# Performance work log

Measured on AMD Instinct MI355X. Metric: run time of the kernel, lower is better.

## Reference

```python
import jax, jax.numpy as jnp
import numpy as np


def conv(x, w, b=None, pad=1):
    y = jax.lax.conv_general_dilated(x, w, (1, 1), [(pad, pad), (pad, pad)],
                                     dimension_numbers=('NCHW', 'OIHW', 'NCHW'))
    if b is not None:
        y = y + b[None, :, None, None]
    return y


def grid_sample(img, gx, gy):
    # bilinear, zeros padding, align_corners=False (torch F.grid_sample default)
    B, C, H, W = img.shape
    ix = ((gx + 1.0) * W - 1.0) * 0.5
    iy = ((gy + 1.0) * H - 1.0) * 0.5
    x0 = jnp.floor(ix)
    y0 = jnp.floor(iy)

    def gather(xi, yi):
        valid = (xi >= 0) & (xi <= W - 1) & (yi >= 0) & (yi <= H - 1)
        xc = jnp.clip(xi, 0, W - 1).astype(jnp.int32)
        yc = jnp.clip(yi, 0, H - 1).astype(jnp.int32)
        b = jnp.arange(B)[:, None, None]
        return img[b, :, yc, xc] * valid[..., None].astype(img.dtype)  # (B,H,W,C)

    wx1 = ix - x0
    wy1 = iy - y0
    wx0 = 1.0 - wx1
    wy0 = 1.0 - wy1
    out = (gather(x0, y0) * (wx0 * wy0)[..., None]
           + gather(x0 + 1, y0) * (wx1 * wy0)[..., None]
           + gather(x0, y0 + 1) * (wx0 * wy1)[..., None]
           + gather(x0 + 1, y0 + 1) * (wx1 * wy1)[..., None])
    return out.transpose(0, 3, 1, 2)  # (B,C,H,W)


def setup_inputs() -> dict:
    key = jax.random.key(0)
    ks = jax.random.split(key, 32)
    B, H, W, hd = 4, 512, 512, 16
    f = lambda k, shp: jax.random.normal(k, shp, dtype=jnp.float32) * 0.05
    z = lambda n: jnp.zeros((n,), dtype=jnp.float32)
    d = {
        'net': f(ks[0], (B, hd, H, W)),
        'inp': f(ks[1], (B, hd, H, W)),
        'corr': f(ks[2], (B, 3, H, W)),
        'noise': f(ks[3], (B, 3, H, W)),
        # BasicMotionEncoder (channels=3, hidden=32, output_dim=64)
        'wc1': f(ks[4], (32, 3, 3, 3)), 'bc1': z(32),
        'wc2': f(ks[5], (32, 32, 3, 3)), 'bc2': z(32),
        'wf1': f(ks[6], (32, 3, 3, 3)), 'bf1': z(32),
        'wf2': f(ks[7], (32, 32, 3, 3)), 'bf2': z(32),
        'we': f(ks[8], (61, 64, 3, 3)), 'be': z(61),
        # SepConvGRU (hidden_size=16, L=4)
        'loc1_w': f(ks[9], (16, 96, 5, 5)), 'loc1_b': z(16),
        'loc2_w': f(ks[10], (8, 16, 5, 5)), 'loc2_b': z(8),
        'wz': f(ks[11], (16, 144, 3, 3)), 'bz': z(16),
        'wr': f(ks[12], (16, 144, 3, 3)), 'br': z(16),
        'wq': f(ks[13], (16, 96, 3, 3)), 'bq': z(16),
        # CBAM (reduction 16 -> mid=1; bias-free, standard impl)
        'ca_w1': f(ks[14], (1, 16, 1, 1)),
        'ca_w2': f(ks[15], (16, 1, 1, 1)),
        'sa_w': f(ks[16], (1, 2, 7, 7)),
        # FlowHead (input 16, hidden 64, out 3)
        'fh1_w': f(ks[17], (64, 16, 3, 3)), 'fh1_b': z(64),
        'fh2_w': f(ks[18], (3, 64, 3, 3)), 'fh2_b': z(3),
    }
    return d


def reference(net, inp, corr, noise, wc1, bc1, wc2, bc2, wf1, bf1, wf2, bf2, we, be,
              loc1_w, loc1_b, loc2_w, loc2_b, wz, bz, wr, br, wq, bq,
              ca_w1, ca_w2, sa_w, fh1_w, fh1_b, fh2_w, fh2_b):
    # --- BasicMotionEncoder ---
    cor = jax.nn.relu(conv(corr, wc1, bc1, 1))
    cor = jax.nn.relu(conv(cor, wc2, bc2, 1))
    flo = jax.nn.relu(conv(noise, wf1, bf1, 1))
    flo = jax.nn.relu(conv(flo, wf2, bf2, 1))
    mo = jax.nn.relu(conv(jnp.concatenate([cor, flo], 1), we, be, 1))
    motion = jnp.concatenate([mo, noise], 1)  # (B,64,H,W)
    x = jnp.concatenate([inp, motion], 1)     # (B,hd+64,H,W)
    h = net
    B, C, H, W = h.shape
    # --- SepConvGRU ---
    t = jax.nn.leaky_relu(conv(jnp.concatenate([x, h], 1), loc1_w, loc1_b, 2), 0.2)
    flows = conv(t, loc2_w, loc2_b, 2)        # (B,2L,H,W)
    L = flows.shape[1] // 2
    flows = flows.reshape(B, L, 2, H, W)
    xx = jnp.arange(W, dtype=h.dtype)[None, None, :]  # (1,1,W)
    yy = jnp.arange(H, dtype=h.dtype)[None, :, None]  # (1,H,1)

    def warp_one(flow):  # flow: (B,2,H,W); warp h by -flow
        vgx = xx - flow[:, 0]
        vgy = yy - flow[:, 1]
        gx = 2.0 * vgx / max(W - 1, 1) - 1.0
        gy = 2.0 * vgy / max(H - 1, 1) - 1.0
        return grid_sample(h, gx, gy)

    wrapped = jax.vmap(warp_one, in_axes=1, out_axes=1)(flows)  # (B,L,C,H,W)
    wrapped = wrapped.reshape(B, L * C, H, W)
    hx = jnp.concatenate([wrapped, x], 1)     # (B,9*hd,H,W)
    zg = jax.nn.sigmoid(conv(hx, wz, bz, 1))
    rg = jax.nn.sigmoid(conv(hx, wr, br, 1))
    q = jnp.tanh(conv(jnp.concatenate([rg * h, x], 1), wq, bq, 1))
    h = (1.0 - zg) * h + zg * q
    # --- CBAM ---
    avg = h.mean((2, 3), keepdims=True)
    mx = h.max((2, 3), keepdims=True)
    mlp = lambda v: conv(jax.nn.relu(conv(v, ca_w1, None, 0)), ca_w2, None, 0)
    h = h * jax.nn.sigmoid(mlp(avg) + mlp(mx))
    sa = jnp.concatenate([h.mean(1, keepdims=True), h.max(1, keepdims=True)], 1)
    h = h * jax.nn.sigmoid(conv(sa, sa_w, None, 3))
    # --- FlowHead ---
    delta_flow = conv(jax.nn.relu(conv(h, fh1_w, fh1_b, 1)), fh2_w, fh2_b, 1)
    return h, delta_flow
```

## Files before the change

### kernel.cpp

```cpp
#include <hip/hip_runtime.h>
#include <hip/hip_bf16.h>
#include <math.h>

using bf16 = __hip_bfloat16;
typedef __attribute__((ext_vector_type(8))) short short8;
typedef __attribute__((ext_vector_type(4))) float f32x4;

__device__ __forceinline__ float b2f(bf16 v){ return __bfloat162float(v); }
__device__ __forceinline__ bf16 f2b(float v){ return __float2bfloat16(v); }
__device__ __forceinline__ float bs2f(short s){
  union{unsigned u; float f;} x; x.u = ((unsigned)(unsigned short)s)<<16; return x.f;
}

template<int A> __device__ __forceinline__ float act_fn(float v){
  if constexpr (A==1) return fmaxf(v, 0.f);
  else if constexpr (A==2) return v > 0.f ? v : 0.2f*v;
  else if constexpr (A==3) return 1.f/(1.f+expf(-v));
  else if constexpr (A==4) return tanhf(v);
  else return v;
}

struct Srcs9 { const bf16* p[9]; int code[9]; };
struct WMap  { int base[9]; int lo[9]; int hi[9]; };

template<int KK, int ACT, int NT>
__global__ __launch_bounds__(256) void conv_mfma(
    Srcs9 S, int Gin, const bf16* __restrict__ flows,
    const bf16* __restrict__ Bw, const float* __restrict__ bias,
    bf16* __restrict__ outS, size_t slabS, float* __restrict__ outF, int Cout,
    int H, int W)
{
  constexpr int TS=16, HALO=TS+KK-1, PAD=KK/2, NPAIR=(KK*KK+1)/2, HH=HALO*HALO;
  constexpr int NMT = (NT==1)?4:((NT==2)?8:16);
  __shared__ __align__(16) bf16 As[2][HH*24];
  const int tid=threadIdx.x, lane=tid&63, wv=tid>>6;
  const int ln=lane&15, gq=lane>>4;
  const int tilesx=W/TS;
  const int tx0=(blockIdx.x%tilesx)*TS, ty0=(blockIdx.x/tilesx)*TS;
  const int b=blockIdx.z; const int HW=H*W;
  int ntile, mt0;
  if constexpr (NT==1){ ntile=0;    mt0=wv*4; }
  else if constexpr (NT==2){ ntile=wv&1; mt0=(wv>>1)*8; }
  else { ntile=wv; mt0=0; }

  f32x4 acc[NMT];
  #pragma unroll
  for (int t=0;t<NMT;++t) acc[t]=(f32x4){0.f,0.f,0.f,0.f};

  const short8 Z8 = {0,0,0,0,0,0,0,0};
  const int px0=tid, px1=tid+256;
  const int hy0=px0/HALO, hx0=px0-hy0*HALO;
  const int hy1=px1/HALO, hx1=px1-hy1*HALO;
  const bool act1 = (px1<HH);
  const int gy0=ty0+hy0-PAD, gx0=tx0+hx0-PAD;
  const int gy1=ty0+hy1-PAD, gx1=tx0+hx1-PAD;
  const bool in0 = (gy0>=0&&gy0<H&&gx0>=0&&gx0<W);
  const bool in1 = act1 && (gy1>=0&&gy1<H&&gx1>=0&&gx1<W);

  auto gather = [&](int g, bool inb, int gy, int gx, short8& A0, short8& A1){
    const int code = S.code[g];
    const bf16* sp = S.p[g];
    if (code == 0) {
      if (inb) {
        const bf16* qp = sp + ((size_t)b*HW + (size_t)gy*W + gx)*16;
        A0 = *(const short8*)qp; A1 = *(const short8*)(qp+8);
      } else { A0 = Z8; A1 = Z8; }
    } else {
      if (inb) {
        const int l = code-1;
        const size_t p = (size_t)b*HW + (size_t)gy*W + gx;
        const unsigned fp_ = *(const unsigned*)(flows + p*16 + 2*l);
        const float fx = bs2f((short)(fp_&0xffff)), fy = bs2f((short)(fp_>>16));
        const float vgx = (float)gx - fx, vgy = (float)gy - fy;
        const float gxn = 2.f*vgx/(float)(W-1) - 1.f;
        const float gyn = 2.f*vgy/(float)(H-1) - 1.f;
        const float ix = ((gxn+1.f)*(float)W - 1.f)*0.5f;
        const float iy = ((gyn+1.f)*(float)H - 1.f)*0.5f;
        const float x0f = floorf(ix), y0f = floorf(iy);
        const float wx1 = ix-x0f, wy1 = iy-y0f, wx0 = 1.f-wx1, wy0 = 1.f-wy1;
        const int x0=(int)x0f, y0=(int)y0f, x1=x0+1, y1=y0+1;
        const bool vx0=(x0>=0)&(x0<W), vx1=(x1>=0)&(x1<W);
        const bool vy0=(y0>=0)&(y0<H), vy1=(y1>=0)&(y1<H);
        const int xc0=min(max(x0,0),W-1), xc1=min(max(x1,0),W-1);
        const int yc0=min(max(y0,0),H-1), yc1=min(max(y1,0),H-1);
        const float w00=wx0*wy0*((vx0&&vy0)?1.f:0.f);
        const float w10=wx1*wy0*((vx1&&vy0)?1.f:0.f);
        const float w01=wx0*wy1*((vx0&&vy1)?1.f:0.f);
        const float w11=wx1*wy1*((vx1&&vy1)?1.f:0.f);
        const bf16* nb = sp + (size_t)b*HW*16;
        const bf16* p00 = nb + ((size_t)yc0*W+xc0)*16;
        const bf16* p10 = nb + ((size_t)yc0*W+xc1)*16;
        const bf16* p01 = nb + ((size_t)yc1*W+xc0)*16;
        const bf16* p11 = nb + ((size_t)yc1*W+xc1)*16;
        const short8 a00=*(const short8*)p00, b00=*(const short8*)(p00+8);
        const short8 a10=*(const short8*)p10, b10=*(const short8*)(p10+8);
        const short8 a01=*(const short8*)p01, b01=*(const short8*)(p01+8);
        const short8 a11=*(const short8*)p11, b11=*(const short8*)(p11+8);
        __align__(16) bf16 tmp[16];
        #pragma unroll
        for (int c=0;c<8;++c){
          tmp[c]   = f2b(w00*bs2f(a00[c]) + w10*bs2f(a10[c]) + w01*bs2f(a01[c]) + w11*bs2f(a11[c]));
          tmp[8+c] = f2b(w00*bs2f(b00[c]) + w10*bs2f(b10[c]) + w01*bs2f(b01[c]) + w11*bs2f(b11[c]));
        }
        A0 = *(const short8*)tmp; A1 = *(const short8*)(tmp+8);
      } else { A0 = Z8; A1 = Z8; }
    }
  };

  auto mfma_g = [&](int g, const bf16* buf){
    #pragma unroll
    for (int p=0;p<NPAIR;++p){
      const short8 bfrag = *(const short8*)(Bw + ((((size_t)g*NPAIR+p)*NT + ntile)*64 + lane)*8);
      int off = 2*p + (gq>>1);
      if (off >= KK*KK) off = 0;
      const int dy = off/KK, dx = off - (off/KK)*KK;
      const int ce = (ln+dx)*24 + ((gq&1)*8);
      #pragma unroll
      for (int t=0;t<NMT;++t){
        const short8 af = *(const short8*)(buf + (size_t)(mt0+t+dy)*HALO*24 + ce);
        acc[t] = __builtin_amdgcn_mfma_f32_16x16x32_bf16(af, bfrag, acc[t], 0, 0, 0);
      }
    }
  };

  for (int g=0; g<Gin; ++g) {
    short8 a0, a1, c0v, c1v;
    gather(g, in0, gy0, gx0, a0, a1);
    if (act1) gather(g, in1, gy1, gx1, c0v, c1v);
    if (g > 0) mfma_g(g-1, As[(g-1)&1]);
    bf16* buf = As[g&1];
    *(short8*)(buf + (size_t)px0*24)     = a0;
    *(short8*)(buf + (size_t)px0*24 + 8) = a1;
    if (act1){
      *(short8*)(buf + (size_t)px1*24)     = c0v;
      *(short8*)(buf + (size_t)px1*24 + 8) = c1v;
    }
    __syncthreads();
  }
  mfma_g(Gin-1, As[(Gin-1)&1]);

  const int co = ntile*16 + ln;
  const float bv = bias[co];
  if (outS) {
    #pragma unroll
    for (int t=0;t<NMT;++t){
      const int y = ty0 + mt0 + t;
      bf16* op = outS + (size_t)ntile*slabS + ((size_t)b*HW + (size_t)y*W + tx0 + gq*4)*16 + ln;
      #pragma unroll
      for (int r=0;r<4;++r) op[(size_t)r*16] = f2b(act_fn<ACT>(acc[t][r] + bv));
    }
  } else {
    if (co < Cout) {
      #pragma unroll
      for (int t=0;t<NMT;++t){
        const int y = ty0 + mt0 + t;
        float4 f;
        f.x = act_fn<ACT>(acc[t][0]+bv); f.y = act_fn<ACT>(acc[t][1]+bv);
        f.z = act_fn<ACT>(acc[t][2]+bv); f.w = act_fn<ACT>(acc[t][3]+bv);
        *(float4*)(outF + ((size_t)b*Cout + co)*HW + (size_t)y*W + tx0 + gq*4) = f;
      }
    }
  }
}

__global__ void prep_w(const float* __restrict__ W1, const float* __restrict__ W2, int coSplit,
                       const float* __restrict__ b1, const float* __restrict__ b2,
                       WMap M, int NPAIR, int NTp, int Cout, int CinO, int T,
                       bf16* __restrict__ Bw, float* __restrict__ bOut, int total)
{
  const int i = blockIdx.x*256 + threadIdx.x;
  if (i < total) {
    const int j=i&7, l=(i>>3)&63, ln2=l&15, gq2=l>>4;
    int r=i>>9; const int nt=r%NTp; r/=NTp; const int p=r%NPAIR; const int g=r/NPAIR;
    const int k=gq2*8+j, off=2*p+(k>>4), ci=k&15, co=nt*16+ln2;
    float w=0.f;
    if (off<T && co<Cout && ci>=M.lo[g] && ci<M.hi[g]) {
      const int cin = M.base[g]+ci;
      if (!W2 || co<coSplit) w = W1[((size_t)co*CinO+cin)*T+off];
      else                   w = W2[((size_t)(co-coSplit)*CinO+cin)*T+off];
    }
    Bw[i] = f2b(w);
  }
  if (i < 64) {
    float bv=0.f;
    if (i<Cout) bv = (!b2 || i<coSplit) ? (b1? b1[i]:0.f) : b2[i-coSplit];
    bOut[i]=bv;
  }
}

__global__ void pack16(const float* __restrict__ src, bf16* __restrict__ dst, int HW){
  const int px = blockIdx.x*256+threadIdx.x; const int b=blockIdx.y;
  if (px>=HW) return;
  __align__(16) bf16 t[16];
  #pragma unroll
  for (int c=0;c<16;++c) t[c]=f2b(src[((size_t)b*16+c)*HW+px]);
  bf16* d = dst + ((size_t)b*HW+px)*16;
  *(short8*)d = *(const short8*)t; *(short8*)(d+8) = *(const short8*)(t+8);
}

__global__ void pack_cn(const float* __restrict__ corr, const float* __restrict__ noise,
                        bf16* __restrict__ dst, int HW){
  const int px = blockIdx.x*256+threadIdx.x; const int b=blockIdx.y;
  if (px>=HW) return;
  __align__(16) bf16 t[16];
  #pragma unroll
  for (int c=0;c<16;++c) t[c]=f2b(0.f);
  #pragma unroll
  for (int c=0;c<3;++c){
    t[c]   = f2b(corr [((size_t)b*3+c)*HW+px]);
    t[3+c] = f2b(noise[((size_t)b*3+c)*HW+px]);
  }
  bf16* d = dst + ((size_t)b*HW+px)*16;
  *(short8*)d = *(const short8*)t; *(short8*)(d+8) = *(const short8*)(t+8);
}

__global__ void noise_tail(const float* __restrict__ noise, bf16* __restrict__ mslab3, int HW){
  const int px = blockIdx.x*256+threadIdx.x; const int b=blockIdx.y;
  if (px>=HW) return;
  bf16* d = mslab3 + ((size_t)b*HW+px)*16;
  #pragma unroll
  for (int c=0;c<3;++c) d[13+c] = f2b(noise[((size_t)b*3+c)*HW+px]);
}

__global__ void rh_k(const bf16* __restrict__ rg, const bf16* __restrict__ netT,
                     bf16* __restrict__ rh, int HW){
  const int px = blockIdx.x*256+threadIdx.x; const int b=blockIdx.y;
  if (px>=HW) return;
  const size_t base = ((size_t)b*HW+px)*16;
  const short8 r0=*(const short8*)(rg+base),  r1=*(const short8*)(rg+base+8);
  const short8 n0=*(const short8*)(netT+base), n1=*(const short8*)(netT+base+8);
  __align__(16) bf16 t[16];
  #pragma unroll
  for (int c=0;c<8;++c){
    t[c]   = f2b(bs2f(r0[c])*bs2f(n0[c]));
    t[8+c] = f2b(bs2f(r1[c])*bs2f(n1[c]));
  }
  *(short8*)(rh+base) = *(const short8*)t; *(short8*)(rh+base+8) = *(const short8*)(t+8);
}

__global__ void h1_k(const bf16* __restrict__ zg, const bf16* __restrict__ q,
                     const float* __restrict__ net, bf16* __restrict__ hT, int HW){
  const int px = blockIdx.x*256+threadIdx.x; const int b=blockIdx.y;
  if (px>=HW) return;
  const size_t base = ((size_t)b*HW+px)*16;
  const short8 z0=*(const short8*)(zg+base), z1=*(const short8*)(zg+base+8);
  const short8 q0=*(const short8*)(q+base),  q1=*(const short8*)(q+base+8);
  __align__(16) bf16 t[16];
  #pragma unroll
  for (int c=0;c<8;++c){
    const float za=bs2f(z0[c]), zb=bs2f(z1[c]);
    const float na=net[((size_t)b*16+c)*HW+px], nb2=net[((size_t)b*16+8+c)*HW+px];
    t[c]   = f2b((1.f-za)*na + za*bs2f(q0[c]));
    t[8+c] = f2b((1.f-zb)*nb2 + zb*bs2f(q1[c]));
  }
  *(short8*)(hT+base) = *(const short8*)t; *(short8*)(hT+base+8) = *(const short8*)(t+8);
}

__global__ __launch_bounds__(256) void castats_p1(const bf16* __restrict__ hT,
                                                  float* __restrict__ part, int HW){
  const int blk=blockIdx.x, b=blockIdx.y;
  const int per = HW>>5;
  const bf16* base = hT + ((size_t)b*HW + (size_t)blk*per)*16;
  float s[16], m[16];
  #pragma unroll
  for (int c=0;c<16;++c){ s[c]=0.f; m[c]=-3.4e38f; }
  for (int i=threadIdx.x;i<per;i+=256){
    const short8 a=*(const short8*)(base+(size_t)i*16);
    const short8 bb=*(const short8*)(base+(size_t)i*16+8);
    #pragma unroll
    for (int c=0;c<8;++c){
      const float v=bs2f(a[c]);  s[c]+=v;   m[c]=fmaxf(m[c],v);
      const float w=bs2f(bb[c]); s[8+c]+=w; m[8+c]=fmaxf(m[8+c],w);
    }
  }
  #pragma unroll
  for (int o=32;o>=1;o>>=1){
    #pragma unroll
    for (int c=0;c<16;++c){ s[c]+=__shfl_down(s[c],o); m[c]=fmaxf(m[c],__shfl_down(m[c],o)); }
  }
  __shared__ float ls[4][16], lm[4][16];
  const int w4=threadIdx.x>>6;
  if ((threadIdx.x&63)==0){
    #pragma unroll
    for (int c=0;c<16;++c){ ls[w4][c]=s[c]; lm[w4][c]=m[c]; }
  }
  __syncthreads();
  if (threadIdx.x<16){
    const int c=threadIdx.x;
    part[((size_t)(b*32+blk))*32 + c]      = ls[0][c]+ls[1][c]+ls[2][c]+ls[3][c];
    part[((size_t)(b*32+blk))*32 + 16 + c] = fmaxf(fmaxf(lm[0][c],lm[1][c]),fmaxf(lm[2][c],lm[3][c]));
  }
}

__global__ void castats_p2(const float* __restrict__ part, float* __restrict__ stats, int HW){
  const int t = threadIdx.x; if (t>=64) return;
  const int b=t>>4, c=t&15;
  float s=0.f, m=-3.4e38f;
  for (int k=0;k<32;++k){
    s += part[((size_t)(b*32+k))*32 + c];
    m  = fmaxf(m, part[((size_t)(b*32+k))*32 + 16 + c]);
  }
  stats[t*2]=s/(float)HW; stats[t*2+1]=m;
}

__global__ void cascale_k(const float* __restrict__ stats, const float* __restrict__ w1,
                          const float* __restrict__ w2, float* __restrict__ scale){
  const int t = threadIdx.x; if (t>=64) return;
  const int c = t & 15;
  float pa = w1[c]*stats[t*2], pm = w1[c]*stats[t*2+1];
  #pragma unroll
  for (int o=8;o>=1;o>>=1){ pa += __shfl_xor(pa,o,16); pm += __shfl_xor(pm,o,16); }
  const float y = w2[c]*fmaxf(pa,0.f) + w2[c]*fmaxf(pm,0.f);
  scale[t] = 1.f/(1.f+expf(-y));
}

__global__ void sastats_k(const bf16* __restrict__ hT, const float* __restrict__ scale,
                          bf16* __restrict__ sa2, int HW){
  const int px = blockIdx.x*256+threadIdx.x; const int b=blockIdx.y;
  if (px>=HW) return;
  const size_t base = ((size_t)b*HW+px)*16;
  const short8 a=*(const short8*)(hT+base), c8=*(const short8*)(hT+base+8);
  float s=0.f, m=-3.4e38f;
  #pragma unroll
  for (int c=0;c<8;++c){
    const float v=bs2f(a[c])*scale[b*16+c];    s+=v; m=fmaxf(m,v);
    const float w=bs2f(c8[c])*scale[b*16+8+c]; s+=w; m=fmaxf(m,w);
  }
  sa2[((size_t)b*2+0)*HW+px] = f2b(s*(1.f/16.f));
  sa2[((size_t)b*2+1)*HW+px] = f2b(m);
}

__global__ __launch_bounds__(256) void saconv_k(const bf16* __restrict__ sa2,
    const float* __restrict__ w, bf16* __restrict__ samap, int H, int W){
  __shared__ float wl[98];
  if (threadIdx.x < 98) wl[threadIdx.x] = w[threadIdx.x];
  __syncthreads();
  const int i = blockIdx.x*256 + threadIdx.x; const int b = blockIdx.y;
  const int HW = H*W;
  if (i >= HW) return;
  const int y = i / W, x = i - (i/W)*W;
  float s = 0.f;
  #pragma unroll
  for (int ch=0; ch<2; ++ch){
    const size_t base = ((size_t)b*2+ch)*HW;
    for (int ky=0;ky<7;++ky){
      const int yy=y+ky-3; if (yy<0||yy>=H) continue;
      for (int kx=0;kx<7;++kx){
        const int xx=x+kx-3; if (xx<0||xx>=W) continue;
        s += b2f(sa2[base+(size_t)yy*W+xx]) * wl[ch*49+ky*7+kx];
      }
    }
  }
  samap[(size_t)b*HW+i] = f2b(1.f/(1.f+expf(-s)));
}

__global__ void hfinal_k(bf16* __restrict__ hT, const float* __restrict__ scale,
                         const bf16* __restrict__ samap, float* __restrict__ outh, int HW){
  const int px = blockIdx.x*256+threadIdx.x; const int b=blockIdx.y;
  if (px>=HW) return;
  const float sa = b2f(samap[(size_t)b*HW+px]);
  const size_t base = ((size_t)b*HW+px)*16;
  const short8 a=*(const short8*)(hT+base), c8=*(const short8*)(hT+base+8);
  __align__(16) bf16 t[16];
  #pragma unroll
  for (int c=0;c<8;++c){
    const float v=bs2f(a[c])*scale[b*16+c]*sa;
    const float w=bs2f(c8[c])*scale[b*16+8+c]*sa;
    t[c]=f2b(v); t[8+c]=f2b(w);
    outh[((size_t)b*16+c)*HW+px]=v; outh[((size_t)b*16+8+c)*HW+px]=w;
  }
  *(short8*)(hT+base)=*(const short8*)t; *(short8*)(hT+base+8)=*(const short8*)(t+8);
}

extern "C" void kernel_launch(void* const* d_in, const int* in_sizes, int n_in,
                              void* d_out, int out_size, void* d_ws, size_t ws_size,
                              hipStream_t stream)
{
  const float* net   = (const float*)d_in[0];
  const float* inp   = (const float*)d_in[1];
  const float* corr  = (const float*)d_in[2];
  const float* noise = (const float*)d_in[3];
  const float* wc1 = (const float*)d_in[4];  const float* bc1 = (const float*)d_in[5];
  const float* wc2 = (const float*)d_in[6];  const float* bc2 = (const float*)d_in[7];
  const float* wf1 = (const float*)d_in[8];  const float* bf1 = (const float*)d_in[9];
  const float* wf2 = (const float*)d_in[10]; const float* bf2 = (const float*)d_in[11];
  const float* we  = (const float*)d_in[12]; const float* be  = (const float*)d_in[13];
  const float* loc1_w = (const float*)d_in[14]; const float* loc1_b = (const float*)d_in[15];
  const float* loc2_w = (const float*)d_in[16]; const float* loc2_b = (const float*)d_in[17];
  const float* wz = (const float*)d_in[18]; const float* bz = (const float*)d_in[19];
  const float* wr = (const float*)d_in[20]; const float* br = (const float*)d_in[21];
  const float* wq = (const float*)d_in[22]; const float* bq = (const float*)d_in[23];
  const float* ca_w1 = (const float*)d_in[24]; const float* ca_w2 = (const float*)d_in[25];
  const float* sa_w  = (const float*)d_in[26];
  const float* fh1_w = (const float*)d_in[27]; const float* fh1_b = (const float*)d_in[28];
  const float* fh2_w = (const float*)d_in[29]; const float* fh2_b = (const float*)d_in[30];

  const int B = 4, H = 512, W = 512, HW = H*W;
  const size_t U  = 32ull<<20;
  const size_t SS = (size_t)B*HW*16;
  char* ws = (char*)d_ws;

  bf16* cor1   = (bf16*)(ws + 0*U);
  bf16* flo1   = (bf16*)(ws + 2*U);
  bf16* flo2   = (bf16*)(ws + 4*U);
  bf16* cnoise = (bf16*)(ws + 6*U);
  bf16* motion = (bf16*)(ws + 0*U);
  bf16* inpT   = (bf16*)(ws + 4*U);
  bf16* tbuf   = (bf16*)(ws + 5*U);
  bf16* netT   = (bf16*)(ws + 6*U);
  bf16* flows  = (bf16*)(ws + 7*U);
  bf16* rh     = (bf16*)(ws + 5*U);
  bf16* qb     = (bf16*)(ws + 6*U);
  bf16* hT     = (bf16*)(ws + 5*U);
  bf16* fh1o   = (bf16*)(ws + 0*U);
  float* part    = (float*)(ws + 4*U);
  float* stats   = (float*)(ws + 4*U + (64<<10));
  float* scale   = (float*)(ws + 4*U + (128<<10));
  bf16*  sa2     = (bf16*)(ws + 4*U + (1<<20));
  bf16*  samap   = (bf16*)(ws + 4*U + (6<<20));
  bf16*  Bw_fh2  = (bf16*)(ws + 4*U + (16<<20));
  float* bias_fh2= (float*)(ws + 4*U + (17<<20));

  float* out_h  = (float*)d_out;
  float* out_df = out_h + (size_t)B*16*HW;
  bf16*  cor2   = (bf16*)d_out;
  bf16*  zgrg   = (bf16*)d_out;
  bf16*  BwAll  = (bf16*)out_df;
  float* biasAll= (float*)(BwAll + 190464);

  const size_t oCor1=0, oCor2=5120, oFlo1=15360, oFlo2=20480, oMo=30720,
               oLoc1=71680, oLoc2=111616, oZgrg=118272, oQ=164352, oFh1=179712;

  const dim3 pgrid((HW+255)/256, B);
  const dim3 cgrid((W/16)*(H/16), 1, B);

  auto WM = [](int b0,int b1,int b2,int b3,int b4,int b5,int b6,int b7,int b8,
               int lo0,int hi0)->WMap{
    WMap m{};
    const int bs[9]={b0,b1,b2,b3,b4,b5,b6,b7,b8};
    for (int g=0; g<9; ++g){ m.base[g]=bs[g]; m.lo[g]=0; m.hi[g]=16; }
    m.lo[0]=lo0; m.hi[0]=hi0;
    return m;
  };

  #define PREP(W1,W2,SPL,B1,B2,MAP,NP,NTP,CO,CIN,T,BWOFF,BIDX) \
    { const int tot = 0; (void)tot; \
      const int total = ((BWOFF##_G)*(NP)*(NTP))*512; \
      prep_w<<<(total+255)/256,256,0,stream>>>(W1,W2,SPL,B1,B2,MAP,NP,NTP,CO,CIN,T, \
        BwAll+BWOFF, biasAll+BIDX*64, total); }

  { const int G=1, NP=5, NTP=2, total=G*NP*NTP*512;
    prep_w<<<(total+255)/256,256,0,stream>>>(wc1,nullptr,0,bc1,nullptr,
      WM(0,0,0,0,0,0,0,0,0, 0,3), NP,NTP,32,3,9, BwAll+oCor1, biasAll+0*64, total); }
  { const int G=2, NP=5, NTP=2, total=G*NP*NTP*512;
    prep_w<<<(total+255)/256,256,0,stream>>>(wc2,nullptr,0,bc2,nullptr,
      WM(0,16,0,0,0,0,0,0,0, 0,16), NP,NTP,32,32,9, BwAll+oCor2, biasAll+1*64, total); }
  { const int G=1, NP=5, NTP=2, total=G*NP*NTP*512;
    prep_w<<<(total+255)/256,256,0,stream>>>(wf1,nullptr,0,bf1,nullptr,
      WM(-3,0,0,0,0,0,0,0,0, 3,6), NP,NTP,32,3,9, BwAll+oFlo1, biasAll+2*64, total); }
  { const int G=2, NP=5, NTP=2, total=G*NP*NTP*512;
    prep_w<<<(total+255)/256,256,0,stream>>>(wf2,nullptr,0,bf2,nullptr,
      WM(0,16,0,0,0,0,0,0,0, 0,16), NP,NTP,32,32,9, BwAll+oFlo2, biasAll+3*64, total); }
  { const int G=4, NP=5, NTP=4, total=G*NP*NTP*512;
    prep_w<<<(total+255)/256,256,0,stream>>>(we,nullptr,0,be,nullptr,
      WM(0,16,32,48,0,0,0,0,0, 0,16), NP,NTP,61,64,9, BwAll+oMo, biasAll+4*64, total); }
  { const int G=6, NP=13, NTP=1, total=G*NP*NTP*512;
    prep_w<<<(total+255)/256,256,0,stream>>>(loc1_w,nullptr,0,loc1_b,nullptr,
      WM(0,16,32,48,64,80,0,0,0, 0,16), NP,NTP,16,96,25, BwAll+oLoc1, biasAll+5*64, total); }
  { const int G=1, NP=13, NTP=1, total=G*NP*NTP*512;
    prep_w<<<(total+255)/256,256,0,stream>>>(loc2_w,nullptr,0,loc2_b,nullptr,
      WM(0,0,0,0,0,0,0,0,0, 0,16), NP,NTP,8,16,25, BwAll+oLoc2, biasAll+6*64, total); }
  { const int G=9, NP=5, NTP=2, total=G*NP*NTP*512;
    prep_w<<<(total+255)/256,256,0,stream>>>(wz,wr,16,bz,br,
      WM(0,16,32,48,64,80,96,112,128, 0,16), NP,NTP,32,144,9, BwAll+oZgrg, biasAll+7*64, total); }
  { const int G=6, NP=5, NTP=1, total=G*NP*NTP*512;
    prep_w<<<(total+255)/256,256,0,stream>>>(wq,nullptr,0,bq,nullptr,
      WM(0,16,32,48,64,80,0,0,0, 0,16), NP,NTP,16,96,9, BwAll+oQ, biasAll+8*64, total); }
  { const int G=1, NP=5, NTP=4, total=G*NP*NTP*512;
    prep_w<<<(total+255)/256,256,0,stream>>>(fh1_w,nullptr,0,fh1_b,nullptr,
      WM(0,0,0,0,0,0,0,0,0, 0,16), NP,NTP,64,16,9, BwAll+oFh1, biasAll+9*64, total); }

  pack_cn<<<pgrid,256,0,stream>>>(corr, noise, cnoise, HW);
  { Srcs9 S{}; S.p[0]=cnoise; S.code[0]=0;
    conv_mfma<3,1,2><<<cgrid,256,0,stream>>>(S,1,nullptr,BwAll+oCor1,biasAll+0*64,cor1,SS,nullptr,32,H,W); }
  { Srcs9 S{}; S.p[0]=cor1; S.p[1]=cor1+SS;
    conv_mfma<3,1,2><<<cgrid,256,0,stream>>>(S,2,nullptr,BwAll+oCor2,biasAll+1*64,cor2,SS,nullptr,32,H,W); }
  { Srcs9 S{}; S.p[0]=cnoise;
    conv_mfma<3,1,2><<<cgrid,256,0,stream>>>(S,1,nullptr,BwAll+oFlo1,biasAll+2*64,flo1,SS,nullptr,32,H,W); }
  { Srcs9 S{}; S.p[0]=flo1; S.p[1]=flo1+SS;
    conv_mfma<3,1,2><<<cgrid,256,0,stream>>>(S,2,nullptr,BwAll+oFlo2,biasAll+3*64,flo2,SS,nullptr,32,H,W); }
  { Srcs9 S{}; S.p[0]=cor2; S.p[1]=cor2+SS; S.p[2]=flo2; S.p[3]=flo2+SS;
    conv_mfma<3,1,4><<<cgrid,256,0,stream>>>(S,4,nullptr,BwAll+oMo,biasAll+4*64,motion,SS,nullptr,61,H,W); }
  noise_tail<<<pgrid,256,0,stream>>>(noise, motion+3*SS, HW);

  pack16<<<pgrid,256,0,stream>>>(inp, inpT, HW);
  pack16<<<pgrid,256,0,stream>>>(net, netT, HW);

  { Srcs9 S{}; S.p[0]=inpT; S.p[1]=motion; S.p[2]=motion+SS; S.p[3]=motion+2*SS; S.p[4]=motion+3*SS; S.p[5]=netT;
    conv_mfma<5,2,1><<<cgrid,256,0,stream>>>(S,6,nullptr,BwAll+oLoc1,biasAll+5*64,tbuf,SS,nullptr,16,H,W); }
  { Srcs9 S{}; S.p[0]=tbuf;
    conv_mfma<5,0,1><<<cgrid,256,0,stream>>>(S,1,nullptr,BwAll+oLoc2,biasAll+6*64,flows,SS,nullptr,8,H,W); }

  { Srcs9 S{};
    S.p[0]=netT; S.code[0]=1; S.p[1]=netT; S.code[1]=2;
    S.p[2]=netT; S.code[2]=3; S.p[3]=netT; S.code[3]=4;
    S.p[4]=inpT; S.p[5]=motion; S.p[6]=motion+SS; S.p[7]=motion+2*SS; S.p[8]=motion+3*SS;
    conv_mfma<3,3,2><<<cgrid,256,0,stream>>>(S,9,flows,BwAll+oZgrg,biasAll+7*64,zgrg,SS,nullptr,32,H,W); }
  rh_k<<<pgrid,256,0,stream>>>(zgrg+SS, netT, rh, HW);
  { Srcs9 S{}; S.p[0]=rh; S.p[1]=inpT; S.p[2]=motion; S.p[3]=motion+SS; S.p[4]=motion+2*SS; S.p[5]=motion+3*SS;
    conv_mfma<3,4,1><<<cgrid,256,0,stream>>>(S,6,nullptr,BwAll+oQ,biasAll+8*64,qb,SS,nullptr,16,H,W); }
  h1_k<<<pgrid,256,0,stream>>>(zgrg, qb, net, hT, HW);

  castats_p1<<<dim3(32,B),256,0,stream>>>(hT, part, HW);
  castats_p2<<<1,64,0,stream>>>(part, stats, HW);
  cascale_k<<<1,64,0,stream>>>(stats, ca_w1, ca_w2, scale);
  sastats_k<<<pgrid,256,0,stream>>>(hT, scale, sa2, HW);
  saconv_k<<<pgrid,256,0,stream>>>(sa2, sa_w, samap, H, W);
  hfinal_k<<<pgrid,256,0,stream>>>(hT, scale, samap, out_h, HW);

  { const int G=4, NP=5, NTP=1, total=G*NP*NTP*512;
    prep_w<<<(total+255)/256,256,0,stream>>>(fh2_w,nullptr,0,fh2_b,nullptr,
      WM(0,16,32,48,0,0,0,0,0, 0,16), NP,NTP,3,64,9, Bw_fh2, bias_fh2, total); }
  { Srcs9 S{}; S.p[0]=hT;
    conv_mfma<3,1,4><<<cgrid,256,0,stream>>>(S,1,nullptr,BwAll+oFh1,biasAll+9*64,fh1o,SS,nullptr,64,H,W); }
  { Srcs9 S{}; S.p[0]=fh1o; S.p[1]=fh1o+SS; S.p[2]=fh1o+2*SS; S.p[3]=fh1o+3*SS;
    conv_mfma<3,0,1><<<cgrid,256,0,stream>>>(S,4,nullptr,Bw_fh2,bias_fh2,nullptr,SS,out_df,3,H,W); }
}
```

Measured before the change: 1.036 ms.

## Fuse kernels, merge cor1/flo1 convs, batch weight prep, split LDS planes

The two first-layer convs that read the packed corr/noise input become one 64-output conv. All weight-prep launches are batched into a single descriptor-driven kernel, and the three packing kernels become one. The r*h product is computed inside the q-conv gather instead of a separate pass, the CBAM scale kernels are merged, and the spatial-attention conv is fused into the final h kernel. LDS tiles move from an interleaved 24-stride layout to two 8-channel planes, and buffers are reassigned. The aim is fewer launches, fewer global round trips and less LDS padding, at the cost of possible LDS bank conflicts and a more complex prep kernel.

```diff
diff --git a/kernel.cpp b/kernel.cpp
--- a/kernel.cpp
+++ b/kernel.cpp
@@ -21,18 +21,18 @@
 }
 
 struct Srcs9 { const bf16* p[9]; int code[9]; };
-struct WMap  { int base[9]; int lo[9]; int hi[9]; };
 
 template<int KK, int ACT, int NT>
 __global__ __launch_bounds__(256) void conv_mfma(
-    Srcs9 S, int Gin, const bf16* __restrict__ flows,
+    Srcs9 S, int Gin, const bf16* __restrict__ flows, const bf16* __restrict__ rgp,
     const bf16* __restrict__ Bw, const float* __restrict__ bias,
     bf16* __restrict__ outS, size_t slabS, float* __restrict__ outF, int Cout,
     int H, int W)
 {
   constexpr int TS=16, HALO=TS+KK-1, PAD=KK/2, NPAIR=(KK*KK+1)/2, HH=HALO*HALO;
+  constexpr int PL = HH*8;
   constexpr int NMT = (NT==1)?4:((NT==2)?8:16);
-  __shared__ __align__(16) bf16 As[2][HH*24];
+  __shared__ __align__(16) bf16 As[4*PL];
   const int tid=threadIdx.x, lane=tid&63, wv=tid>>6;
   const int ln=lane&15, gq=lane>>4;
   const int tilesx=W/TS;
@@ -64,6 +64,19 @@
       if (inb) {
         const bf16* qp = sp + ((size_t)b*HW + (size_t)gy*W + gx)*16;
         A0 = *(const short8*)qp; A1 = *(const short8*)(qp+8);
+      } else { A0 = Z8; A1 = Z8; }
+    } else if (code == 5) {
+      if (inb) {
+        const size_t base = ((size_t)b*HW + (size_t)gy*W + gx)*16;
+        const short8 n0=*(const short8*)(sp+base),  n1=*(const short8*)(sp+base+8);
+        const short8 r0=*(const short8*)(rgp+base), r1=*(const short8*)(rgp+base+8);
+        __align__(16) bf16 tmp[16];
+        #pragma unroll
+        for (int c=0;c<8;++c){
+          tmp[c]   = f2b(bs2f(r0[c])*bs2f(n0[c]));
+          tmp[8+c] = f2b(bs2f(r1[c])*bs2f(n1[c]));
+        }
+        A0 = *(const short8*)tmp; A1 = *(const short8*)(tmp+8);
       } else { A0 = Z8; A1 = Z8; }
     } else {
       if (inb) {
@@ -108,16 +121,16 @@
   };
 
   auto mfma_g = [&](int g, const bf16* buf){
+    const bf16* pb = buf + (gq&1)*PL;
     #pragma unroll
     for (int p=0;p<NPAIR;++p){
       const short8 bfrag = *(const short8*)(Bw + ((((size_t)g*NPAIR+p)*NT + ntile)*64 + lane)*8);
       int off = 2*p + (gq>>1);
       if (off >= KK*KK) off = 0;
       const int dy = off/KK, dx = off - (off/KK)*KK;
-      const int ce = (ln+dx)*24 + ((gq&1)*8);
       #pragma unroll
       for (int t=0;t<NMT;++t){
-        const short8 af = *(const short8*)(buf + (size_t)(mt0+t+dy)*HALO*24 + ce);
+        const short8 af = *(const short8*)(pb + (size_t)((mt0+t+dy)*HALO + ln + dx)*8);
         acc[t] = __builtin_amdgcn_mfma_f32_16x16x32_bf16(af, bfrag, acc[t], 0, 0, 0);
       }
     }
@@ -127,17 +140,17 @@
     short8 a0, a1, c0v, c1v;
     gather(g, in0, gy0, gx0, a0, a1);
     if (act1) gather(g, in1, gy1, gx1, c0v, c1v);
-    if (g > 0) mfma_g(g-1, As[(g-1)&1]);
-    bf16* buf = As[g&1];
-    *(short8*)(buf + (size_t)px0*24)     = a0;
-    *(short8*)(buf + (size_t)px0*24 + 8) = a1;
+    if (g > 0) mfma_g(g-1, As + ((g-1)&1)*2*PL);
+    bf16* buf = As + (g&1)*2*PL;
+    *(short8*)(buf + (size_t)px0*8)      = a0;
+    *(short8*)(buf + PL + (size_t)px0*8) = a1;
     if (act1){
-      *(short8*)(buf + (size_t)px1*24)     = c0v;
-      *(short8*)(buf + (size_t)px1*24 + 8) = c1v;
+      *(short8*)(buf + (size_t)px1*8)      = c0v;
+      *(short8*)(buf + PL + (size_t)px1*8) = c1v;
     }
     __syncthreads();
   }
-  mfma_g(Gin-1, As[(Gin-1)&1]);
+  mfma_g(Gin-1, As + ((Gin-1)&1)*2*PL);
 
   const int co = ntile*16 + ln;
   const float bv = bias[co];
@@ -163,45 +176,50 @@
   }
 }
 
-__global__ void prep_w(const float* __restrict__ W1, const float* __restrict__ W2, int coSplit,
-                       const float* __restrict__ b1, const float* __restrict__ b2,
-                       WMap M, int NPAIR, int NTp, int Cout, int CinO, int T,
-                       bf16* __restrict__ Bw, float* __restrict__ bOut, int total)
-{
+struct PrepDesc {
+  const float *W1, *W2, *b1, *b2;
+  int coSplit, NPAIR, NTp, Cout, CinO, T;
+  int lo0, hi0, d2, lo2, hi2;
+  int base[9];
+  int total;
+};
+struct PrepAll { PrepDesc d[10]; int n; };
+
+__global__ void prep_w(PrepAll P, bf16* __restrict__ Bw, float* __restrict__ bOut, int grand){
   const int i = blockIdx.x*256 + threadIdx.x;
-  if (i < total) {
-    const int j=i&7, l=(i>>3)&63, ln2=l&15, gq2=l>>4;
-    int r=i>>9; const int nt=r%NTp; r/=NTp; const int p=r%NPAIR; const int g=r/NPAIR;
-    const int k=gq2*8+j, off=2*p+(k>>4), ci=k&15, co=nt*16+ln2;
-    float w=0.f;
-    if (off<T && co<Cout && ci>=M.lo[g] && ci<M.hi[g]) {
-      const int cin = M.base[g]+ci;
-      if (!W2 || co<coSplit) w = W1[((size_t)co*CinO+cin)*T+off];
-      else                   w = W2[((size_t)(co-coSplit)*CinO+cin)*T+off];
-    }
-    Bw[i] = f2b(w);
-  }
-  if (i < 64) {
+  if (i < P.n*64) {
+    const int c=i>>6, t=i&63; const PrepDesc& D=P.d[c];
     float bv=0.f;
-    if (i<Cout) bv = (!b2 || i<coSplit) ? (b1? b1[i]:0.f) : b2[i-coSplit];
-    bOut[i]=bv;
-  }
-}
-
-__global__ void pack16(const float* __restrict__ src, bf16* __restrict__ dst, int HW){
+    if (t < D.Cout) bv = (!D.b2 || t < D.coSplit) ? D.b1[t] : D.b2[t-D.coSplit];
+    bOut[c*64+t]=bv;
+  }
+  if (i >= grand) return;
+  int c=0, off0=0;
+  while (i >= off0 + P.d[c].total) { off0 += P.d[c].total; ++c; }
+  const PrepDesc& D = P.d[c];
+  const int j = i - off0;
+  const int jj=j&7, l=(j>>3)&63, ln2=l&15, gq2=l>>4;
+  int r=j>>9; const int nt=r%D.NTp; r/=D.NTp; const int p=r%D.NPAIR; const int g=r/D.NPAIR;
+  const int k=gq2*8+jj, off=2*p+(k>>4), ci=k&15, co=nt*16+ln2;
+  float w=0.f;
+  if (off<D.T && co<D.Cout) {
+    const int lo = (g==0)?D.lo0:0, hi=(g==0)?D.hi0:16;
+    if (!D.W2 || co < D.coSplit) {
+      if (ci>=lo && ci<hi) w = D.W1[((size_t)co*D.CinO + D.base[g]+ci)*D.T + off];
+    } else {
+      if (ci>=D.lo2 && ci<D.hi2) w = D.W2[((size_t)(co-D.coSplit)*D.CinO + D.base[g]+ci+D.d2)*D.T + off];
+    }
+  }
+  Bw[i] = f2b(w);
+}
+
+__global__ void pack_all(const float* __restrict__ corr, const float* __restrict__ noise,
+                         const float* __restrict__ inp, const float* __restrict__ net,
+                         bf16* __restrict__ cnoise, bf16* __restrict__ inpT,
+                         bf16* __restrict__ netT, int HW){
   const int px = blockIdx.x*256+threadIdx.x; const int b=blockIdx.y;
   if (px>=HW) return;
-  __align__(16) bf16 t[16];
-  #pragma unroll
-  for (int c=0;c<16;++c) t[c]=f2b(src[((size_t)b*16+c)*HW+px]);
-  bf16* d = dst + ((size_t)b*HW+px)*16;
-  *(short8*)d = *(const short8*)t; *(short8*)(d+8) = *(const short8*)(t+8);
-}
-
-__global__ void pack_cn(const float* __restrict__ corr, const float* __restrict__ noise,
-                        bf16* __restrict__ dst, int HW){
-  const int px = blockIdx.x*256+threadIdx.x; const int b=blockIdx.y;
-  if (px>=HW) return;
+  const size_t base = ((size_t)b*HW+px)*16;
   __align__(16) bf16 t[16];
   #pragma unroll
   for (int c=0;c<16;++c) t[c]=f2b(0.f);
@@ -210,8 +228,13 @@
     t[c]   = f2b(corr [((size_t)b*3+c)*HW+px]);
     t[3+c] = f2b(noise[((size_t)b*3+c)*HW+px]);
   }
-  bf16* d = dst + ((size_t)b*HW+px)*16;
-  *(short8*)d = *(const short8*)t; *(short8*)(d+8) = *(const short8*)(t+8);
+  *(short8*)(cnoise+base) = *(const short8*)t; *(short8*)(cnoise+base+8) = *(const short8*)(t+8);
+  #pragma unroll
+  for (int c=0;c<16;++c) t[c]=f2b(inp[((size_t)b*16+c)*HW+px]);
+  *(short8*)(inpT+base) = *(const short8*)t; *(short8*)(inpT+base+8) = *(const short8*)(t+8);
+  #pragma unroll
+  for (int c=0;c<16;++c) t[c]=f2b(net[((size_t)b*16+c)*HW+px]);
+  *(short8*)(netT+base) = *(const short8*)t; *(short8*)(netT+base+8) = *(const short8*)(t+8);
 }
 
 __global__ void noise_tail(const float* __restrict__ noise, bf16* __restrict__ mslab3, int HW){
@@ -220,22 +243,6 @@
   bf16* d = mslab3 + ((size_t)b*HW+px)*16;
   #pragma unroll
   for (int c=0;c<3;++c) d[13+c] = f2b(noise[((size_t)b*3+c)*HW+px]);
-}
-
-__global__ void rh_k(const bf16* __restrict__ rg, const bf16* __restrict__ netT,
-                     bf16* __restrict__ rh, int HW){
-  const int px = blockIdx.x*256+threadIdx.x; const int b=blockIdx.y;
-  if (px>=HW) return;
-  const size_t base = ((size_t)b*HW+px)*16;
-  const short8 r0=*(const short8*)(rg+base),  r1=*(const short8*)(rg+base+8);
-  const short8 n0=*(const short8*)(netT+base), n1=*(const short8*)(netT+base+8);
-  __align__(16) bf16 t[16];
-  #pragma unroll
-  for (int c=0;c<8;++c){
-    t[c]   = f2b(bs2f(r0[c])*bs2f(n0[c]));
-    t[8+c] = f2b(bs2f(r1[c])*bs2f(n1[c]));
-  }
-  *(short8*)(rh+base) = *(const short8*)t; *(short8*)(rh+base+8) = *(const short8*)(t+8);
 }
 
 __global__ void h1_k(const bf16* __restrict__ zg, const bf16* __restrict__ q,
@@ -292,7 +299,8 @@
   }
 }
 
-__global__ void castats_p2(const float* __restrict__ part, float* __restrict__ stats, int HW){
+__global__ void castats_fin(const float* __restrict__ part, const float* __restrict__ w1,
+                            const float* __restrict__ w2, float* __restrict__ scale, int HW){
   const int t = threadIdx.x; if (t>=64) return;
   const int b=t>>4, c=t&15;
   float s=0.f, m=-3.4e38f;
@@ -300,14 +308,7 @@
     s += part[((size_t)(b*32+k))*32 + c];
     m  = fmaxf(m, part[((size_t)(b*32+k))*32 + 16 + c]);
   }
-  stats[t*2]=s/(float)HW; stats[t*2+1]=m;
-}
-
-__global__ void cascale_k(const float* __restrict__ stats, const float* __restrict__ w1,
-                          const float* __restrict__ w2, float* __restrict__ scale){
-  const int t = threadIdx.x; if (t>=64) return;
-  const int c = t & 15;
-  float pa = w1[c]*stats[t*2], pm = w1[c]*stats[t*2+1];
+  float pa = w1[c]*(s/(float)HW), pm = w1[c]*m;
   #pragma unroll
   for (int o=8;o>=1;o>>=1){ pa += __shfl_xor(pa,o,16); pm += __shfl_xor(pm,o,16); }
   const float y = w2[c]*fmaxf(pa,0.f) + w2[c]*fmaxf(pm,0.f);
@@ -330,10 +331,11 @@
   sa2[((size_t)b*2+1)*HW+px] = f2b(m);
 }
 
-__global__ __launch_bounds__(256) void saconv_k(const bf16* __restrict__ sa2,
-    const float* __restrict__ w, bf16* __restrict__ samap, int H, int W){
+__global__ __launch_bounds__(256) void hfinal2(bf16* __restrict__ hT, const float* __restrict__ scale,
+    const bf16* __restrict__ sa2, const float* __restrict__ saw,
+    float* __restrict__ outh, int H, int W){
   __shared__ float wl[98];
-  if (threadIdx.x < 98) wl[threadIdx.x] = w[threadIdx.x];
+  if (threadIdx.x < 98) wl[threadIdx.x] = saw[threadIdx.x];
   __syncthreads();
   const int i = blockIdx.x*256 + threadIdx.x; const int b = blockIdx.y;
   const int HW = H*W;
@@ -351,15 +353,8 @@
       }
     }
   }
-  samap[(size_t)b*HW+i] = f2b(1.f/(1.f+expf(-s)));
-}
-
-__global__ void hfinal_k(bf16* __restrict__ hT, const float* __restrict__ scale,
-                         const bf16* __restrict__ samap, float* __restrict__ outh, int HW){
-  const int px = blockIdx.x*256+threadIdx.x; const int b=blockIdx.y;
-  if (px>=HW) return;
-  const float sa = b2f(samap[(size_t)b*HW+px]);
-  const size_t base = ((size_t)b*HW+px)*16;
+  const float sa = 1.f/(1.f+expf(-s));
+  const size_t base = ((size_t)b*HW+i)*16;
   const short8 a=*(const short8*)(hT+base), c8=*(const short8*)(hT+base+8);
   __align__(16) bf16 t[16];
   #pragma unroll
@@ -367,7 +362,7 @@
     const float v=bs2f(a[c])*scale[b*16+c]*sa;
     const float w=bs2f(c8[c])*scale[b*16+8+c]*sa;
     t[c]=f2b(v); t[8+c]=f2b(w);
-    outh[((size_t)b*16+c)*HW+px]=v; outh[((size_t)b*16+8+c)*HW+px]=w;
+    outh[((size_t)b*16+c)*HW+i]=v; outh[((size_t)b*16+8+c)*HW+i]=w;
   }
   *(short8*)(hT+base)=*(const short8*)t; *(short8*)(hT+base+8)=*(const short8*)(t+8);
 }
@@ -402,127 +397,102 @@
 
   bf16* cor1   = (bf16*)(ws + 0*U);
   bf16* flo1   = (bf16*)(ws + 2*U);
-  bf16* flo2   = (bf16*)(ws + 4*U);
+  bf16* motion = (bf16*)(ws + 0*U);
+  bf16* fh1o   = (bf16*)(ws + 0*U);
+  bf16* inpT   = (bf16*)(ws + 4*U);
+  bf16* flo2   = (bf16*)(ws + 5*U);
+  bf16* flows  = (bf16*)(ws + 5*U);
+  bf16* hT     = (bf16*)(ws + 5*U);
   bf16* cnoise = (bf16*)(ws + 6*U);
-  bf16* motion = (bf16*)(ws + 0*U);
-  bf16* inpT   = (bf16*)(ws + 4*U);
-  bf16* tbuf   = (bf16*)(ws + 5*U);
-  bf16* netT   = (bf16*)(ws + 6*U);
-  bf16* flows  = (bf16*)(ws + 7*U);
-  bf16* rh     = (bf16*)(ws + 5*U);
+  bf16* tbuf   = (bf16*)(ws + 6*U);
   bf16* qb     = (bf16*)(ws + 6*U);
-  bf16* hT     = (bf16*)(ws + 5*U);
-  bf16* fh1o   = (bf16*)(ws + 0*U);
+  bf16* netT   = (bf16*)(ws + 7*U);
   float* part    = (float*)(ws + 4*U);
-  float* stats   = (float*)(ws + 4*U + (64<<10));
-  float* scale   = (float*)(ws + 4*U + (128<<10));
+  float* scale   = (float*)(ws + 4*U + (64<<10));
   bf16*  sa2     = (bf16*)(ws + 4*U + (1<<20));
-  bf16*  samap   = (bf16*)(ws + 4*U + (6<<20));
   bf16*  Bw_fh2  = (bf16*)(ws + 4*U + (16<<20));
   float* bias_fh2= (float*)(ws + 4*U + (17<<20));
 
   float* out_h  = (float*)d_out;
   float* out_df = out_h + (size_t)B*16*HW;
-  bf16*  cor2   = (bf16*)d_out;
   bf16*  zgrg   = (bf16*)d_out;
   bf16*  BwAll  = (bf16*)out_df;
   float* biasAll= (float*)(BwAll + 190464);
 
-  const size_t oCor1=0, oCor2=5120, oFlo1=15360, oFlo2=20480, oMo=30720,
-               oLoc1=71680, oLoc2=111616, oZgrg=118272, oQ=164352, oFh1=179712;
+  const size_t oMrg=0, oCor2=10240, oFlo2=20480, oMo=30720, oLoc1=71680,
+               oLoc2=111616, oZgrg=118272, oQ=164352, oFh1=179712;
+  const int grand = 189952;
 
   const dim3 pgrid((HW+255)/256, B);
   const dim3 cgrid((W/16)*(H/16), 1, B);
 
-  auto WM = [](int b0,int b1,int b2,int b3,int b4,int b5,int b6,int b7,int b8,
-               int lo0,int hi0)->WMap{
-    WMap m{};
-    const int bs[9]={b0,b1,b2,b3,b4,b5,b6,b7,b8};
-    for (int g=0; g<9; ++g){ m.base[g]=bs[g]; m.lo[g]=0; m.hi[g]=16; }
-    m.lo[0]=lo0; m.hi[0]=hi0;
-    return m;
+  auto mk = [](const float* W1, const float* W2, int coSplit, const float* b1, const float* b2,
+               int G, int NP, int NTp, int Cout, int CinO, int T,
+               int lo0, int hi0, int d2, int lo2, int hi2,
+               int b0,int b1_,int b2_,int b3,int b4,int b5,int b6,int b7,int b8)->PrepDesc{
+    PrepDesc d{};
+    d.W1=W1; d.W2=W2; d.b1=b1; d.b2=b2; d.coSplit=coSplit;
+    d.NPAIR=NP; d.NTp=NTp; d.Cout=Cout; d.CinO=CinO; d.T=T;
+    d.lo0=lo0; d.hi0=hi0; d.d2=d2; d.lo2=lo2; d.hi2=hi2;
+    const int bs[9]={b0,b1_,b2_,b3,b4,b5,b6,b7,b8};
+    for (int g=0;g<9;++g) d.base[g]=bs[g];
+    d.total = G*NP*NTp*512;
+    return d;
   };
 
-  #define PREP(W1,W2,SPL,B1,B2,MAP,NP,NTP,CO,CIN,T,BWOFF,BIDX) \
-    { const int tot = 0; (void)tot; \
-      const int total = ((BWOFF##_G)*(NP)*(NTP))*512; \
-      prep_w<<<(total+255)/256,256,0,stream>>>(W1,W2,SPL,B1,B2,MAP,NP,NTP,CO,CIN,T, \
-        BwAll+BWOFF, biasAll+BIDX*64, total); }
-
-  { const int G=1, NP=5, NTP=2, total=G*NP*NTP*512;
-    prep_w<<<(total+255)/256,256,0,stream>>>(wc1,nullptr,0,bc1,nullptr,
-      WM(0,0,0,0,0,0,0,0,0, 0,3), NP,NTP,32,3,9, BwAll+oCor1, biasAll+0*64, total); }
-  { const int G=2, NP=5, NTP=2, total=G*NP*NTP*512;
-    prep_w<<<(total+255)/256,256,0,stream>>>(wc2,nullptr,0,bc2,nullptr,
-      WM(0,16,0,0,0,0,0,0,0, 0,16), NP,NTP,32,32,9, BwAll+oCor2, biasAll+1*64, total); }
-  { const int G=1, NP=5, NTP=2, total=G*NP*NTP*512;
-    prep_w<<<(total+255)/256,256,0,stream>>>(wf1,nullptr,0,bf1,nullptr,
-      WM(-3,0,0,0,0,0,0,0,0, 3,6), NP,NTP,32,3,9, BwAll+oFlo1, biasAll+2*64, total); }
-  { const int G=2, NP=5, NTP=2, total=G*NP*NTP*512;
-    prep_w<<<(total+255)/256,256,0,stream>>>(wf2,nullptr,0,bf2,nullptr,
-      WM(0,16,0,0,0,0,0,0,0, 0,16), NP,NTP,32,32,9, BwAll+oFlo2, biasAll+3*64, total); }
-  { const int G=4, NP=5, NTP=4, total=G*NP*NTP*512;
-    prep_w<<<(total+255)/256,256,0,stream>>>(we,nullptr,0,be,nullptr,
-      WM(0,16,32,48,0,0,0,0,0, 0,16), NP,NTP,61,64,9, BwAll+oMo, biasAll+4*64, total); }
-  { const int G=6, NP=13, NTP=1, total=G*NP*NTP*512;
-    prep_w<<<(total+255)/256,256,0,stream>>>(loc1_w,nullptr,0,loc1_b,nullptr,
-      WM(0,16,32,48,64,80,0,0,0, 0,16), NP,NTP,16,96,25, BwAll+oLoc1, biasAll+5*64, total); }
-  { const int G=1, NP=13, NTP=1, total=G*NP*NTP*512;
-    prep_w<<<(total+255)/256,256,0,stream>>>(loc2_w,nullptr,0,loc2_b,nullptr,
-      WM(0,0,0,0,0,0,0,0,0, 0,16), NP,NTP,8,16,25, BwAll+oLoc2, biasAll+6*64, total); }
-  { const int G=9, NP=5, NTP=2, total=G*NP*NTP*512;
-    prep_w<<<(total+255)/256,256,0,stream>>>(wz,wr,16,bz,br,
-      WM(0,16,32,48,64,80,96,112,128, 0,16), NP,NTP,32,144,9, BwAll+oZgrg, biasAll+7*64, total); }
-  { const int G=6, NP=5, NTP=1, total=G*NP*NTP*512;
-    prep_w<<<(total+255)/256,256,0,stream>>>(wq,nullptr,0,bq,nullptr,
-      WM(0,16,32,48,64,80,0,0,0, 0,16), NP,NTP,16,96,9, BwAll+oQ, biasAll+8*64, total); }
-  { const int G=1, NP=5, NTP=4, total=G*NP*NTP*512;
-    prep_w<<<(total+255)/256,256,0,stream>>>(fh1_w,nullptr,0,fh1_b,nullptr,
-      WM(0,0,0,0,0,0,0,0,0, 0,16), NP,NTP,64,16,9, BwAll+oFh1, biasAll+9*64, total); }
-
-  pack_cn<<<pgrid,256,0,stream>>>(corr, noise, cnoise, HW);
-  { Srcs9 S{}; S.p[0]=cnoise; S.code[0]=0;
-    conv_mfma<3,1,2><<<cgrid,256,0,stream>>>(S,1,nullptr,BwAll+oCor1,biasAll+0*64,cor1,SS,nullptr,32,H,W); }
+  {
+    PrepAll P{}; P.n = 9;
+    P.d[0] = mk(wc1, wf1, 32, bc1, bf1, 1,5,4, 64,3,9,  0,3, -3,3,6, 0,0,0,0,0,0,0,0,0);
+    P.d[1] = mk(wc2, nullptr,0, bc2,nullptr, 2,5,2, 32,32,9, 0,16, 0,0,16, 0,16,0,0,0,0,0,0,0);
+    P.d[2] = mk(wf2, nullptr,0, bf2,nullptr, 2,5,2, 32,32,9, 0,16, 0,0,16, 0,16,0,0,0,0,0,0,0);
+    P.d[3] = mk(we,  nullptr,0, be, nullptr, 4,5,4, 61,64,9, 0,16, 0,0,16, 0,16,32,48,0,0,0,0,0);
+    P.d[4] = mk(loc1_w,nullptr,0, loc1_b,nullptr, 6,13,1, 16,96,25, 0,16, 0,0,16, 0,16,32,48,64,80,0,0,0);
+    P.d[5] = mk(loc2_w,nullptr,0, loc2_b,nullptr, 1,13,1, 8,16,25,  0,16, 0,0,16, 0,0,0,0,0,0,0,0,0);
+    P.d[6] = mk(wz, wr, 16, bz, br, 9,5,2, 32,144,9, 0,16, 0,0,16, 0,16,32,48,64,80,96,112,128);
+    P.d[7] = mk(wq, nullptr,0, bq, nullptr, 6,5,1, 16,96,9, 0,16, 0,0,16, 0,16,32,48,64,80,0,0,0);
+    P.d[8] = mk(fh1_w,nullptr,0, fh1_b,nullptr, 1,5,4, 64,16,9, 0,16, 0,0,16, 0,0,0,0,0,0,0,0,0);
+    prep_w<<<(grand+255)/256,256,0,stream>>>(P, BwAll, biasAll, grand);
+  }
+
+  pack_all<<<pgrid,256,0,stream>>>(corr, noise, inp, net, cnoise, inpT, netT, HW);
+
+  { Srcs9 S{}; S.p[0]=cnoise;
+    conv_mfma<3,1,4><<<cgrid,256,0,stream>>>(S,1,nullptr,nullptr,BwAll+oMrg,biasAll+0*64,cor1,SS,nullptr,64,H,W); }
   { Srcs9 S{}; S.p[0]=cor1; S.p[1]=cor1+SS;
-    conv_mfma<3,1,2><<<cgrid,256,0,stream>>>(S,2,nullptr,BwAll+oCor2,biasAll+1*64,cor2,SS,nullptr,32,H,W); }
-  { Srcs9 S{}; S.p[0]=cnoise;
-    conv_mfma<3,1,2><<<cgrid,256,0,stream>>>(S,1,nullptr,BwAll+oFlo1,biasAll+2*64,flo1,SS,nullptr,32,H,W); }
+    conv_mfma<3,1,2><<<cgrid,256,0,stream>>>(S,2,nullptr,nullptr,BwAll+oCor2,biasAll+1*64,zgrg,SS,nullptr,32,H,W); }
   { Srcs9 S{}; S.p[0]=flo1; S.p[1]=flo1+SS;
-    conv_mfma<3,1,2><<<cgrid,256,0,stream>>>(S,2,nullptr,BwAll+oFlo2,biasAll+3*64,flo2,SS,nullptr,32,H,W); }
-  { Srcs9 S{}; S.p[0]=cor2; S.p[1]=cor2+SS; S.p[2]=flo2; S.p[3]=flo2+SS;
-    conv_mfma<3,1,4><<<cgrid,256,0,stream>>>(S,4,nullptr,BwAll+oMo,biasAll+4*64,motion,SS,nullptr,61,H,W); }
+    conv_mfma<3,1,2><<<cgrid,256,0,stream>>>(S,2,nullptr,nullptr,BwAll+oFlo2,biasAll+2*64,flo2,SS,nullptr,32,H,W); }
+  { Srcs9 S{}; S.p[0]=zgrg; S.p[1]=zgrg+SS; S.p[2]=flo2; S.p[3]=flo2+SS;
+    conv_mfma<3,1,4><<<cgrid,256,0,stream>>>(S,4,nullptr,nullptr,BwAll+oMo,biasAll+3*64,motion,SS,nullptr,61,H,W); }
   noise_tail<<<pgrid,256,0,stream>>>(noise, motion+3*SS, HW);
 
-  pack16<<<pgrid,256,0,stream>>>(inp, inpT, HW);
-  pack16<<<pgrid,256,0,stream>>>(net, netT, HW);
-
   { Srcs9 S{}; S.p[0]=inpT; S.p[1]=motion; S.p[2]=motion+SS; S.p[3]=motion+2*SS; S.p[4]=motion+3*SS; S.p[5]=netT;
-    conv_mfma<5,2,1><<<cgrid,256,0,stream>>>(S,6,nullptr,BwAll+oLoc1,biasAll+5*64,tbuf,SS,nullptr,16,H,W); }
+    conv_mfma<5,2,1><<<cgrid,256,0,stream>>>(S,6,nullptr,nullptr,BwAll+oLoc1,biasAll+4*64,tbuf,SS,nullptr,16,H,W); }
   { Srcs9 S{}; S.p[0]=tbuf;
-    conv_mfma<5,0,1><<<cgrid,256,0,stream>>>(S,1,nullptr,BwAll+oLoc2,biasAll+6*64,flows,SS,nullptr,8,H,W); }
+    conv_mfma<5,0,1><<<cgrid,256,0,stream>>>(S,1,nullptr,nullptr,BwAll+oLoc2,biasAll+5*64,flows,SS,nullptr,8,H,W); }
 
   { Srcs9 S{};
     S.p[0]=netT; S.code[0]=1; S.p[1]=netT; S.code[1]=2;
     S.p[2]=netT; S.code[2]=3; S.p[3]=netT; S.code[3]=4;
     S.p[4]=inpT; S.p[5]=motion; S.p[6]=motion+SS; S.p[7]=motion+2*SS; S.p[8]=motion+3*SS;
-    conv_mfma<3,3,2><<<cgrid,256,0,stream>>>(S,9,flows,BwAll+oZgrg,biasAll+7*64,zgrg,SS,nullptr,32,H,W); }
-  rh_k<<<pgrid,256,0,stream>>>(zgrg+SS, netT, rh, HW);
-  { Srcs9 S{}; S.p[0]=rh; S.p[1]=inpT; S.p[2]=motion; S.p[3]=motion+SS; S.p[4]=motion+2*SS; S.p[5]=motion+3*SS;
-    conv_mfma<3,4,1><<<cgrid,256,0,stream>>>(S,6,nullptr,BwAll+oQ,biasAll+8*64,qb,SS,nullptr,16,H,W); }
+    conv_mfma<3,3,2><<<cgrid,256,0,stream>>>(S,9,flows,nullptr,BwAll+oZgrg,biasAll+6*64,zgrg,SS,nullptr,32,H,W); }
+  { Srcs9 S{};
+    S.p[0]=netT; S.code[0]=5;
+    S.p[1]=inpT; S.p[2]=motion; S.p[3]=motion+SS; S.p[4]=motion+2*SS; S.p[5]=motion+3*SS;
+    conv_mfma<3,4,1><<<cgrid,256,0,stream>>>(S,6,nullptr,zgrg+SS,BwAll+oQ,biasAll+7*64,qb,SS,nullptr,16,H,W); }
   h1_k<<<pgrid,256,0,stream>>>(zgrg, qb, net, hT, HW);
 
+  { PrepAll P{}; P.n = 1;
+    P.d[0] = mk(fh2_w,nullptr,0, fh2_b,nullptr, 4,5,1, 3,64,9, 0,16, 0,0,16, 0,16,32,48,0,0,0,0,0);
+    prep_w<<<(10240+255)/256,256,0,stream>>>(P, Bw_fh2, bias_fh2, 10240); }
+
   castats_p1<<<dim3(32,B),256,0,stream>>>(hT, part, HW);
-  castats_p2<<<1,64,0,stream>>>(part, stats, HW);
-  cascale_k<<<1,64,0,stream>>>(stats, ca_w1, ca_w2, scale);
+  castats_fin<<<1,64,0,stream>>>(part, ca_w1, ca_w2, scale, HW);
   sastats_k<<<pgrid,256,0,stream>>>(hT, scale, sa2, HW);
-  saconv_k<<<pgrid,256,0,stream>>>(sa2, sa_w, samap, H, W);
-  hfinal_k<<<pgrid,256,0,stream>>>(hT, scale, samap, out_h, HW);
-
-  { const int G=4, NP=5, NTP=1, total=G*NP*NTP*512;
-    prep_w<<<(total+255)/256,256,0,stream>>>(fh2_w,nullptr,0,fh2_b,nullptr,
-      WM(0,16,32,48,0,0,0,0,0, 0,16), NP,NTP,3,64,9, Bw_fh2, bias_fh2, total); }
+  hfinal2<<<pgrid,256,0,stream>>>(hT, scale, sa2, sa_w, out_h, H, W);
+
   { Srcs9 S{}; S.p[0]=hT;
-    conv_mfma<3,1,4><<<cgrid,256,0,stream>>>(S,1,nullptr,BwAll+oFh1,biasAll+9*64,fh1o,SS,nullptr,64,H,W); }
+    conv_mfma<3,1,4><<<cgrid,256,0,stream>>>(S,1,nullptr,nullptr,BwAll+oFh1,biasAll+8*64,fh1o,SS,nullptr,64,H,W); }
   { Srcs9 S{}; S.p[0]=fh1o; S.p[1]=fh1o+SS; S.p[2]=fh1o+2*SS; S.p[3]=fh1o+3*SS;
-    conv_mfma<3,0,1><<<cgrid,256,0,stream>>>(S,4,nullptr,Bw_fh2,bias_fh2,nullptr,SS,out_df,3,H,W); }
-}
+    conv_mfma<3,0,1><<<cgrid,256,0,stream>>>(S,4,nullptr,nullptr,Bw_fh2,bias_fh2,nullptr,SS,out_df,3,H,W); }
+}
```

Result: slower. 1.215 ms (+17.2%).
